# Kernel optimization log

Measured on AMD Instinct MI355X. Metric: run time of the kernel, lower is better.

The kernel has to match this reference:

```python
import jax, jax.numpy as jnp
import numpy as np

EPS = 1e-06
B, N, D, K, C = 16, 256, 4, 10, 100  # batch, nodes, pseudo dim, kernels, out_channels


def setup_inputs() -> dict:
    key = jax.random.key(0)
    k1, k2, k3, k4, k5, k6 = jax.random.split(key, 6)
    stdv = np.sqrt(6.0 / (K + D))
    x = jax.random.normal(k1, (B, N, K * C), dtype=jnp.float32)
    adj = (jax.random.uniform(k2, (B, N, N)) > 0.5).astype(jnp.float32)
    pseudo = jax.random.uniform(k3, (B, N, N, D), dtype=jnp.float32)
    mu = jax.random.uniform(k4, (K, D), minval=-stdv, maxval=stdv, dtype=jnp.float32)
    sigma = jax.random.uniform(k5, (K, D), minval=-stdv, maxval=stdv, dtype=jnp.float32)
    lim = 1.0 / np.sqrt(C)
    W = jax.random.uniform(k6, (C, C), minval=-lim, maxval=lim, dtype=jnp.float32)
    b = jnp.zeros((C,), dtype=jnp.float32)
    return {"x": x, "adj": adj, "pseudo": pseudo, "mu": mu, "sigma": sigma, "W": W, "b": b}


def reference(x, adj, pseudo, mu, sigma, W, b):
    # Gaussian kernel edge weights: [B,N,N,K]
    diff = pseudo[..., None, :] - mu            # [B,N,N,K,D]
    g = jnp.exp(jnp.sum(-0.5 * diff ** 2 / (EPS + sigma ** 2), axis=-1))
    ag = g * adj[..., None]                     # adjacency-masked weights [B,N,N,K]
    xk = x.reshape(B, N, K, C) @ W.T + b        # per-kernel linear  [B,N,K,C]
    # res[b,k,c,n] = sum_m ag[b,n,m,k] * xk[b,m,k,c]
    res = jnp.einsum('bnmk,bmkc->bkcn', ag, xk)
    return res.reshape(B, K * C, N)
```

## Files before the change

kernel.cpp:

```cpp
#include <hip/hip_runtime.h>

typedef __bf16 bf16;
typedef __attribute__((ext_vector_type(4)))  __bf16 bf16x4;
typedef __attribute__((ext_vector_type(8)))  __bf16 bf16x8;
typedef __attribute__((ext_vector_type(4)))  float  f32x4;
typedef __attribute__((ext_vector_type(16))) float  f32x16;

constexpr int B_ = 16, N_ = 256, K_ = 10, C_ = 100, CP_ = 112;
constexpr float NL2E = -0.7213475204444817f;
constexpr int BF_SLICE = 16 * 2 * 128 * 8;

__device__ inline bf16x8 cvt8(const float* p) {
    float4 a = *(const float4*)p, b = *(const float4*)(p + 4);
    bf16x8 r = {(bf16)a.x, (bf16)a.y, (bf16)a.z, (bf16)a.w,
                (bf16)b.x, (bf16)b.y, (bf16)b.z, (bf16)b.w};
    return r;
}
__device__ inline bf16x8 cvt4z(const float* p) {
    float4 a = *(const float4*)p;
    bf16x8 r = {(bf16)a.x, (bf16)a.y, (bf16)a.z, (bf16)a.w,
                (bf16)0.0f, (bf16)0.0f, (bf16)0.0f, (bf16)0.0f};
    return r;
}

__global__ __launch_bounds__(256, 4) void xk_gemm(
    const float* __restrict__ x, const float* __restrict__ W,
    const float* __restrict__ bias, bf16* __restrict__ xkT)
{
    __shared__ float xs[32 * 101 + 16];

    const int bid = blockIdx.x;
    const int xcd = bid & 7, s = bid >> 3;
    const int b  = xcd + 8 * (s / 80);
    const int rr = s % 80, kk = rr >> 3, mq = rr & 7;
    const int tid = threadIdx.x;
    const int w = tid >> 6, l = tid & 63, l31 = l & 31, h = l >> 5;
    const int c = w * 32 + l31;

    const float* xb = x + ((size_t)(b * N_ + mq * 32) * K_ + kk) * C_;
    #pragma unroll 4
    for (int idx = tid; idx < 800; idx += 256) {
        int row = idx / 25, q = idx - row * 25;
        float4 v = *(const float4*)(xb + (size_t)row * (K_ * C_) + q * 4);
        *(float4*)(&xs[row * 101 + q * 4]) = v;
    }

    const bf16x8 zf = {(bf16)0.f,(bf16)0.f,(bf16)0.f,(bf16)0.f,
                       (bf16)0.f,(bf16)0.f,(bf16)0.f,(bf16)0.f};

    bf16x8 af[7];
    const float* Wrow = W + (size_t)c * C_;
    #pragma unroll
    for (int js = 0; js < 7; ++js) {
        const int jb = js * 16 + h * 8;
        af[js] = zf;
        if (c < C_) {
            if (jb + 8 <= C_)      af[js] = cvt8(Wrow + jb);
            else if (jb < C_)      af[js] = cvt4z(Wrow + jb);
        }
    }

    f32x16 acc;
    #pragma unroll
    for (int r = 0; r < 16; ++r) {
        int crow = w * 32 + (r & 3) + 8 * (r >> 2) + 4 * h;
        acc[r] = (crow < C_) ? bias[crow] : 0.0f;
    }

    __syncthreads();

    #pragma unroll
    for (int js = 0; js < 7; ++js) {
        const int jb = js * 16 + h * 8;
        bf16x8 b0 = zf;
        if (jb < C_) b0 = cvt8(&xs[l31 * 101 + jb]);
        acc = __builtin_amdgcn_mfma_f32_32x32x16_bf16(af[js], b0, acc, 0, 0, 0);
    }

    bf16* op = xkT + (size_t)(b * K_ + kk) * BF_SLICE;
    const int mg = mq * 32 + l31;
    const int base = (((mg >> 4) << 1) + ((mg >> 3) & 1)) * 1024 + (mg & 7);
    #pragma unroll
    for (int r = 0; r < 16; ++r) {
        const int crow = w * 32 + (r & 3) + 8 * (r >> 2) + 4 * h;
        op[base + crow * 8] = (bf16)acc[r];
    }
}

__global__ __launch_bounds__(256, 4) void gauss_agg(
    const float* __restrict__ adj, const float* __restrict__ pseudo,
    const float* __restrict__ mu, const float* __restrict__ sigma,
    const bf16* __restrict__ xkT, float* __restrict__ out)
{
    __shared__ __align__(16) char lds[32 * 512];

    const int bid = blockIdx.x;
    const int xcd = bid & 7, s = bid >> 3;
    const int b  = xcd + 8 * (s / 80);
    const int rr = s % 80, kk = rr >> 3, nh = rr & 7;
    const int n32 = nh * 32;
    const int tid = threadIdx.x;
    const int w = tid >> 6, l = tid & 63, l31 = l & 31, h = l >> 5;

    float Av[4], Bv[4], ga = 0.0f;
    #pragma unroll
    for (int d = 0; d < 4; ++d) {
        float sg = sigma[kk * 4 + d];
        float al = NL2E / (1e-6f + sg * sg);
        float mv = mu[kk * 4 + d];
        Av[d] = al; Bv[d] = -2.0f * al * mv; ga += al * mv * mv;
    }

    const float* pbase = pseudo + (size_t)(b * N_ + n32) * N_ * 4;
    const float* abase = adj    + (size_t)(b * N_ + n32) * N_;
    #pragma unroll
    for (int i = 0; i < 8; ++i) {
        const int row = i * 4 + w;
        const float4* pr = (const float4*)(pbase + (size_t)row * N_ * 4);
        const float*  ar = abase + (size_t)row * N_;
        float4 p0 = pr[l];
        float4 p1 = pr[l + 64];
        float4 p2 = pr[l + 128];
        float4 p3 = pr[l + 192];
        float a0 = ar[l], a1 = ar[l + 64], a2 = ar[l + 128], a3 = ar[l + 192];

        float s0 = ga + Av[0]*p0.x*p0.x + Bv[0]*p0.x + Av[1]*p0.y*p0.y + Bv[1]*p0.y
                      + Av[2]*p0.z*p0.z + Bv[2]*p0.z + Av[3]*p0.w*p0.w + Bv[3]*p0.w;
        float s1 = ga + Av[0]*p1.x*p1.x + Bv[0]*p1.x + Av[1]*p1.y*p1.y + Bv[1]*p1.y
                      + Av[2]*p1.z*p1.z + Bv[2]*p1.z + Av[3]*p1.w*p1.w + Bv[3]*p1.w;
        float s2 = ga + Av[0]*p2.x*p2.x + Bv[0]*p2.x + Av[1]*p2.y*p2.y + Bv[1]*p2.y
                      + Av[2]*p2.z*p2.z + Bv[2]*p2.z + Av[3]*p2.w*p2.w + Bv[3]*p2.w;
        float s3 = ga + Av[0]*p3.x*p3.x + Bv[0]*p3.x + Av[1]*p3.y*p3.y + Bv[1]*p3.y
                      + Av[2]*p3.z*p3.z + Bv[2]*p3.z + Av[3]*p3.w*p3.w + Bv[3]*p3.w;

        float g0 = __builtin_amdgcn_exp2f(s0) * a0;
        float g1 = __builtin_amdgcn_exp2f(s1) * a1;
        float g2 = __builtin_amdgcn_exp2f(s2) * a2;
        float g3 = __builtin_amdgcn_exp2f(s3) * a3;

        #pragma unroll
        for (int t = 0; t < 4; ++t) {
            const int m  = l + 64 * t;
            const int ch = m >> 3, half = (m >> 2) & 1, pos = m & 3;
            const float gv = (t == 0) ? g0 : (t == 1) ? g1 : (t == 2) ? g2 : g3;
            *(bf16*)(lds + row * 512 + ((ch ^ (row & 7)) * 16) + half * 8 + pos * 2)
                = (bf16)gv;
        }
    }
    __syncthreads();

    const bf16* bsl = xkT + (size_t)(b * K_ + kk) * BF_SLICE
                          + (size_t)(w * 32 + l31) * 8;
    f32x16 acc;
    #pragma unroll
    for (int i = 0; i < 16; ++i) acc[i] = 0.0f;

    #pragma unroll
    for (int ks = 0; ks < 16; ++ks) {
        bf16x8 af = *(const bf16x8*)(lds + l31 * 512 + (((ks * 2 + h) ^ (l31 & 7)) * 16));
        bf16x8 bf = *(const bf16x8*)(bsl + (size_t)(ks * 2 + h) * 1024);
        acc = __builtin_amdgcn_mfma_f32_32x32x16_bf16(af, bf, acc, 0, 0, 0);
    }

    const int c = w * 32 + l31;
    if (c < C_) {
        float* ob = out + (size_t)(b * K_ + kk) * C_ * N_ + (size_t)c * N_ + n32;
        #pragma unroll
        for (int q = 0; q < 4; ++q) {
            float4 v = {acc[4*q+0], acc[4*q+1], acc[4*q+2], acc[4*q+3]};
            *(float4*)(ob + 8 * q + 4 * h) = v;
        }
    }
}

extern "C" void kernel_launch(void* const* d_in, const int* in_sizes, int n_in,
                              void* d_out, int out_size, void* d_ws, size_t ws_size,
                              hipStream_t stream)
{
    const float* x      = (const float*)d_in[0];
    const float* adj    = (const float*)d_in[1];
    const float* pseudo = (const float*)d_in[2];
    const float* mu     = (const float*)d_in[3];
    const float* sigma  = (const float*)d_in[4];
    const float* W      = (const float*)d_in[5];
    const float* bias   = (const float*)d_in[6];
    float* out = (float*)d_out;
    bf16* xkT  = (bf16*)d_ws;

    hipLaunchKernelGGL(xk_gemm, dim3(1280), dim3(256), 0, stream, x, W, bias, xkT);
    hipLaunchKernelGGL(gauss_agg, dim3(1280), dim3(256), 0, stream,
                       adj, pseudo, mu, sigma, xkT, out);
}
```

Baseline: 33.62 us.

## Process two Gaussian kernels per block in gauss_agg to reuse pseudo/adj loads

Each gauss_agg block now handles two kernel indices (k and k+5), so the pseudo and adj tiles are loaded once and used for both weight matrices, with two LDS buffers and two MFMA accumulators. The grid halves to 640 blocks and the launch bound drops to 2 blocks per SM. This cuts redundant global reads of the large pseudo tensor. In exchange it uses more registers and LDS per block and launches fewer blocks, which lowers parallelism.

```diff
diff --git a/kernel.cpp b/kernel.cpp
--- a/kernel.cpp
+++ b/kernel.cpp
@@ -87,28 +87,32 @@
     }
 }
 
-__global__ __launch_bounds__(256, 4) void gauss_agg(
+__global__ __launch_bounds__(256, 2) void gauss_agg(
     const float* __restrict__ adj, const float* __restrict__ pseudo,
     const float* __restrict__ mu, const float* __restrict__ sigma,
     const bf16* __restrict__ xkT, float* __restrict__ out)
 {
-    __shared__ __align__(16) char lds[32 * 512];
+    __shared__ __align__(16) char lds0[32 * 512];
+    __shared__ __align__(16) char lds1[32 * 512];
 
     const int bid = blockIdx.x;
     const int xcd = bid & 7, s = bid >> 3;
-    const int b  = xcd + 8 * (s / 80);
-    const int rr = s % 80, kk = rr >> 3, nh = rr & 7;
+    const int b  = xcd + 8 * (s / 40);
+    const int rr = s % 40, kp = rr >> 3, nh = rr & 7;
+    const int k0 = kp, k1 = kp + 5;
     const int n32 = nh * 32;
     const int tid = threadIdx.x;
     const int w = tid >> 6, l = tid & 63, l31 = l & 31, h = l >> 5;
 
-    float Av[4], Bv[4], ga = 0.0f;
+    float A0[4], B0[4], g0c = 0.0f, A1[4], B1[4], g1c = 0.0f;
     #pragma unroll
     for (int d = 0; d < 4; ++d) {
-        float sg = sigma[kk * 4 + d];
-        float al = NL2E / (1e-6f + sg * sg);
-        float mv = mu[kk * 4 + d];
-        Av[d] = al; Bv[d] = -2.0f * al * mv; ga += al * mv * mv;
+        float sg0 = sigma[k0 * 4 + d], mv0 = mu[k0 * 4 + d];
+        float al0 = NL2E / (1e-6f + sg0 * sg0);
+        A0[d] = al0; B0[d] = -2.0f * al0 * mv0; g0c += al0 * mv0 * mv0;
+        float sg1 = sigma[k1 * 4 + d], mv1 = mu[k1 * 4 + d];
+        float al1 = NL2E / (1e-6f + sg1 * sg1);
+        A1[d] = al1; B1[d] = -2.0f * al1 * mv1; g1c += al1 * mv1 * mv1;
     }
 
     const float* pbase = pseudo + (size_t)(b * N_ + n32) * N_ * 4;
@@ -124,51 +128,70 @@
         float4 p3 = pr[l + 192];
         float a0 = ar[l], a1 = ar[l + 64], a2 = ar[l + 128], a3 = ar[l + 192];
 
-        float s0 = ga + Av[0]*p0.x*p0.x + Bv[0]*p0.x + Av[1]*p0.y*p0.y + Bv[1]*p0.y
-                      + Av[2]*p0.z*p0.z + Bv[2]*p0.z + Av[3]*p0.w*p0.w + Bv[3]*p0.w;
-        float s1 = ga + Av[0]*p1.x*p1.x + Bv[0]*p1.x + Av[1]*p1.y*p1.y + Bv[1]*p1.y
-                      + Av[2]*p1.z*p1.z + Bv[2]*p1.z + Av[3]*p1.w*p1.w + Bv[3]*p1.w;
-        float s2 = ga + Av[0]*p2.x*p2.x + Bv[0]*p2.x + Av[1]*p2.y*p2.y + Bv[1]*p2.y
-                      + Av[2]*p2.z*p2.z + Bv[2]*p2.z + Av[3]*p2.w*p2.w + Bv[3]*p2.w;
-        float s3 = ga + Av[0]*p3.x*p3.x + Bv[0]*p3.x + Av[1]*p3.y*p3.y + Bv[1]*p3.y
-                      + Av[2]*p3.z*p3.z + Bv[2]*p3.z + Av[3]*p3.w*p3.w + Bv[3]*p3.w;
-
-        float g0 = __builtin_amdgcn_exp2f(s0) * a0;
-        float g1 = __builtin_amdgcn_exp2f(s1) * a1;
-        float g2 = __builtin_amdgcn_exp2f(s2) * a2;
-        float g3 = __builtin_amdgcn_exp2f(s3) * a3;
+        float q0x = p0.x*p0.x, q0y = p0.y*p0.y, q0z = p0.z*p0.z, q0w = p0.w*p0.w;
+        float q1x = p1.x*p1.x, q1y = p1.y*p1.y, q1z = p1.z*p1.z, q1w = p1.w*p1.w;
+        float q2x = p2.x*p2.x, q2y = p2.y*p2.y, q2z = p2.z*p2.z, q2w = p2.w*p2.w;
+        float q3x = p3.x*p3.x, q3y = p3.y*p3.y, q3z = p3.z*p3.z, q3w = p3.w*p3.w;
+
+        float s00 = g0c + A0[0]*q0x + B0[0]*p0.x + A0[1]*q0y + B0[1]*p0.y
+                        + A0[2]*q0z + B0[2]*p0.z + A0[3]*q0w + B0[3]*p0.w;
+        float s01 = g0c + A0[0]*q1x + B0[0]*p1.x + A0[1]*q1y + B0[1]*p1.y
+                        + A0[2]*q1z + B0[2]*p1.z + A0[3]*q1w + B0[3]*p1.w;
+        float s02 = g0c + A0[0]*q2x + B0[0]*p2.x + A0[1]*q2y + B0[1]*p2.y
+                        + A0[2]*q2z + B0[2]*p2.z + A0[3]*q2w + B0[3]*p2.w;
+        float s03 = g0c + A0[0]*q3x + B0[0]*p3.x + A0[1]*q3y + B0[1]*p3.y
+                        + A0[2]*q3z + B0[2]*p3.z + A0[3]*q3w + B0[3]*p3.w;
+
+        float s10 = g1c + A1[0]*q0x + B1[0]*p0.x + A1[1]*q0y + B1[1]*p0.y
+                        + A1[2]*q0z + B1[2]*p0.z + A1[3]*q0w + B1[3]*p0.w;
+        float s11 = g1c + A1[0]*q1x + B1[0]*p1.x + A1[1]*q1y + B1[1]*p1.y
+                        + A1[2]*q1z + B1[2]*p1.z + A1[3]*q1w + B1[3]*p1.w;
+        float s12 = g1c + A1[0]*q2x + B1[0]*p2.x + A1[1]*q2y + B1[1]*p2.y
+                        + A1[2]*q2z + B1[2]*p2.z + A1[3]*q2w + B1[3]*p2.w;
+        float s13 = g1c + A1[0]*q3x + B1[0]*p3.x + A1[1]*q3y + B1[1]*p3.y
+                        + A1[2]*q3z + B1[2]*p3.z + A1[3]*q3w + B1[3]*p3.w;
 
         #pragma unroll
         for (int t = 0; t < 4; ++t) {
             const int m  = l + 64 * t;
             const int ch = m >> 3, half = (m >> 2) & 1, pos = m & 3;
-            const float gv = (t == 0) ? g0 : (t == 1) ? g1 : (t == 2) ? g2 : g3;
-            *(bf16*)(lds + row * 512 + ((ch ^ (row & 7)) * 16) + half * 8 + pos * 2)
-                = (bf16)gv;
+            const int off = row * 512 + ((ch ^ (row & 7)) * 16) + half * 8 + pos * 2;
+            const float av = (t == 0) ? a0 : (t == 1) ? a1 : (t == 2) ? a2 : a3;
+            const float sA = (t == 0) ? s00 : (t == 1) ? s01 : (t == 2) ? s02 : s03;
+            const float sB = (t == 0) ? s10 : (t == 1) ? s11 : (t == 2) ? s12 : s13;
+            *(bf16*)(lds0 + off) = (bf16)(__builtin_amdgcn_exp2f(sA) * av);
+            *(bf16*)(lds1 + off) = (bf16)(__builtin_amdgcn_exp2f(sB) * av);
         }
     }
     __syncthreads();
 
-    const bf16* bsl = xkT + (size_t)(b * K_ + kk) * BF_SLICE
-                          + (size_t)(w * 32 + l31) * 8;
-    f32x16 acc;
-    #pragma unroll
-    for (int i = 0; i < 16; ++i) acc[i] = 0.0f;
+    const bf16* bsl0 = xkT + (size_t)(b * K_ + k0) * BF_SLICE + (size_t)(w * 32 + l31) * 8;
+    const bf16* bsl1 = xkT + (size_t)(b * K_ + k1) * BF_SLICE + (size_t)(w * 32 + l31) * 8;
+    f32x16 acc0, acc1;
+    #pragma unroll
+    for (int i = 0; i < 16; ++i) { acc0[i] = 0.0f; acc1[i] = 0.0f; }
 
     #pragma unroll
     for (int ks = 0; ks < 16; ++ks) {
-        bf16x8 af = *(const bf16x8*)(lds + l31 * 512 + (((ks * 2 + h) ^ (l31 & 7)) * 16));
-        bf16x8 bf = *(const bf16x8*)(bsl + (size_t)(ks * 2 + h) * 1024);
-        acc = __builtin_amdgcn_mfma_f32_32x32x16_bf16(af, bf, acc, 0, 0, 0);
+        const int aoff = l31 * 512 + (((ks * 2 + h) ^ (l31 & 7)) * 16);
+        bf16x8 af0 = *(const bf16x8*)(lds0 + aoff);
+        bf16x8 af1 = *(const bf16x8*)(lds1 + aoff);
+        bf16x8 bf0 = *(const bf16x8*)(bsl0 + (size_t)(ks * 2 + h) * 1024);
+        bf16x8 bf1 = *(const bf16x8*)(bsl1 + (size_t)(ks * 2 + h) * 1024);
+        acc0 = __builtin_amdgcn_mfma_f32_32x32x16_bf16(af0, bf0, acc0, 0, 0, 0);
+        acc1 = __builtin_amdgcn_mfma_f32_32x32x16_bf16(af1, bf1, acc1, 0, 0, 0);
     }
 
     const int c = w * 32 + l31;
     if (c < C_) {
-        float* ob = out + (size_t)(b * K_ + kk) * C_ * N_ + (size_t)c * N_ + n32;
+        float* ob0 = out + (size_t)(b * K_ + k0) * C_ * N_ + (size_t)c * N_ + n32;
+        float* ob1 = out + (size_t)(b * K_ + k1) * C_ * N_ + (size_t)c * N_ + n32;
         #pragma unroll
         for (int q = 0; q < 4; ++q) {
-            float4 v = {acc[4*q+0], acc[4*q+1], acc[4*q+2], acc[4*q+3]};
-            *(float4*)(ob + 8 * q + 4 * h) = v;
+            float4 v0 = {acc0[4*q+0], acc0[4*q+1], acc0[4*q+2], acc0[4*q+3]};
+            float4 v1 = {acc1[4*q+0], acc1[4*q+1], acc1[4*q+2], acc1[4*q+3]};
+            *(float4*)(ob0 + 8 * q + 4 * h) = v0;
+            *(float4*)(ob1 + 8 * q + 4 * h) = v1;
         }
     }
 }
@@ -188,6 +211,6 @@
     bf16* xkT  = (bf16*)d_ws;
 
     hipLaunchKernelGGL(xk_gemm, dim3(1280), dim3(256), 0, stream, x, W, bias, xkT);
-    hipLaunchKernelGGL(gauss_agg, dim3(1280), dim3(256), 0, stream,
+    hipLaunchKernelGGL(gauss_agg, dim3(640), dim3(256), 0, stream,
                        adj, pseudo, mu, sigma, xkT, out);
 }
```

New measurement: 34.40 us. 2.3% more time.

## Fuse per-kernel linear projection into Gaussian aggregation kernel

Applied to the files above, without the earlier changes.

Merges the xk GEMM and the Gaussian-weighted aggregation into one kernel. Each block now recomputes the projected x tile for all 256 source nodes in shared memory, chunk by chunk, and consumes it right away. This removes the global bf16 intermediate and the second launch. In exchange, the projection and the x reads are repeated 8x across node-tile blocks, and two barriers are added per chunk.

```diff
diff --git a/kernel.cpp b/kernel.cpp
--- a/kernel.cpp
+++ b/kernel.cpp
@@ -6,9 +6,8 @@
 typedef __attribute__((ext_vector_type(4)))  float  f32x4;
 typedef __attribute__((ext_vector_type(16))) float  f32x16;
 
-constexpr int B_ = 16, N_ = 256, K_ = 10, C_ = 100, CP_ = 112;
+constexpr int B_ = 16, N_ = 256, K_ = 10, C_ = 100;
 constexpr float NL2E = -0.7213475204444817f;
-constexpr int BF_SLICE = 16 * 2 * 128 * 8;
 
 __device__ inline bf16x8 cvt8(const float* p) {
     float4 a = *(const float4*)p, b = *(const float4*)(p + 4);
@@ -23,27 +22,24 @@
     return r;
 }
 
-__global__ __launch_bounds__(256, 4) void xk_gemm(
-    const float* __restrict__ x, const float* __restrict__ W,
-    const float* __restrict__ bias, bf16* __restrict__ xkT)
+__global__ __launch_bounds__(256, 4) void fused_gauss(
+    const float* __restrict__ x, const float* __restrict__ adj,
+    const float* __restrict__ pseudo, const float* __restrict__ mu,
+    const float* __restrict__ sigma, const float* __restrict__ W,
+    const float* __restrict__ bias, float* __restrict__ out)
 {
     __shared__ float xs[32 * 101 + 16];
+    __shared__ bf16  xkc[4 * 128 * 8];
+    __shared__ __align__(16) char agb[32 * 512];
 
     const int bid = blockIdx.x;
     const int xcd = bid & 7, s = bid >> 3;
     const int b  = xcd + 8 * (s / 80);
-    const int rr = s % 80, kk = rr >> 3, mq = rr & 7;
+    const int rr = s % 80, kk = rr >> 3, nh = rr & 7;
+    const int n32 = nh * 32;
     const int tid = threadIdx.x;
     const int w = tid >> 6, l = tid & 63, l31 = l & 31, h = l >> 5;
     const int c = w * 32 + l31;
-
-    const float* xb = x + ((size_t)(b * N_ + mq * 32) * K_ + kk) * C_;
-    #pragma unroll 4
-    for (int idx = tid; idx < 800; idx += 256) {
-        int row = idx / 25, q = idx - row * 25;
-        float4 v = *(const float4*)(xb + (size_t)row * (K_ * C_) + q * 4);
-        *(float4*)(&xs[row * 101 + q * 4]) = v;
-    }
 
     const bf16x8 zf = {(bf16)0.f,(bf16)0.f,(bf16)0.f,(bf16)0.f,
                        (bf16)0.f,(bf16)0.f,(bf16)0.f,(bf16)0.f};
@@ -59,48 +55,12 @@
             else if (jb < C_)      af[js] = cvt4z(Wrow + jb);
         }
     }
-
-    f32x16 acc;
+    float bv[16];
     #pragma unroll
     for (int r = 0; r < 16; ++r) {
         int crow = w * 32 + (r & 3) + 8 * (r >> 2) + 4 * h;
-        acc[r] = (crow < C_) ? bias[crow] : 0.0f;
+        bv[r] = (crow < C_) ? bias[crow] : 0.0f;
     }
-
-    __syncthreads();
-
-    #pragma unroll
-    for (int js = 0; js < 7; ++js) {
-        const int jb = js * 16 + h * 8;
-        bf16x8 b0 = zf;
-        if (jb < C_) b0 = cvt8(&xs[l31 * 101 + jb]);
-        acc = __builtin_amdgcn_mfma_f32_32x32x16_bf16(af[js], b0, acc, 0, 0, 0);
-    }
-
-    bf16* op = xkT + (size_t)(b * K_ + kk) * BF_SLICE;
-    const int mg = mq * 32 + l31;
-    const int base = (((mg >> 4) << 1) + ((mg >> 3) & 1)) * 1024 + (mg & 7);
-    #pragma unroll
-    for (int r = 0; r < 16; ++r) {
-        const int crow = w * 32 + (r & 3) + 8 * (r >> 2) + 4 * h;
-        op[base + crow * 8] = (bf16)acc[r];
-    }
-}
-
-__global__ __launch_bounds__(256, 4) void gauss_agg(
-    const float* __restrict__ adj, const float* __restrict__ pseudo,
-    const float* __restrict__ mu, const float* __restrict__ sigma,
-    const bf16* __restrict__ xkT, float* __restrict__ out)
-{
-    __shared__ __align__(16) char lds[32 * 512];
-
-    const int bid = blockIdx.x;
-    const int xcd = bid & 7, s = bid >> 3;
-    const int b  = xcd + 8 * (s / 80);
-    const int rr = s % 80, kk = rr >> 3, nh = rr & 7;
-    const int n32 = nh * 32;
-    const int tid = threadIdx.x;
-    const int w = tid >> 6, l = tid & 63, l31 = l & 31, h = l >> 5;
 
     float Av[4], Bv[4], ga = 0.0f;
     #pragma unroll
@@ -143,31 +103,61 @@
             const int m  = l + 64 * t;
             const int ch = m >> 3, half = (m >> 2) & 1, pos = m & 3;
             const float gv = (t == 0) ? g0 : (t == 1) ? g1 : (t == 2) ? g2 : g3;
-            *(bf16*)(lds + row * 512 + ((ch ^ (row & 7)) * 16) + half * 8 + pos * 2)
+            *(bf16*)(agb + row * 512 + ((ch ^ (row & 7)) * 16) + half * 8 + pos * 2)
                 = (bf16)gv;
         }
     }
+
+    f32x16 acc2;
+    #pragma unroll
+    for (int i = 0; i < 16; ++i) acc2[i] = 0.0f;
+
     __syncthreads();
 
-    const bf16* bsl = xkT + (size_t)(b * K_ + kk) * BF_SLICE
-                          + (size_t)(w * 32 + l31) * 8;
-    f32x16 acc;
-    #pragma unroll
-    for (int i = 0; i < 16; ++i) acc[i] = 0.0f;
+    #pragma unroll 1
+    for (int it = 0; it < 8; ++it) {
+        const float* xb = x + ((size_t)(b * N_ + it * 32) * K_ + kk) * C_;
+        #pragma unroll 4
+        for (int idx = tid; idx < 800; idx += 256) {
+            int row = idx / 25, q = idx - row * 25;
+            float4 v = *(const float4*)(xb + (size_t)row * (K_ * C_) + q * 4);
+            *(float4*)(&xs[row * 101 + q * 4]) = v;
+        }
+        __syncthreads();
 
-    #pragma unroll
-    for (int ks = 0; ks < 16; ++ks) {
-        bf16x8 af = *(const bf16x8*)(lds + l31 * 512 + (((ks * 2 + h) ^ (l31 & 7)) * 16));
-        bf16x8 bf = *(const bf16x8*)(bsl + (size_t)(ks * 2 + h) * 1024);
-        acc = __builtin_amdgcn_mfma_f32_32x32x16_bf16(af, bf, acc, 0, 0, 0);
+        f32x16 acc;
+        #pragma unroll
+        for (int r = 0; r < 16; ++r) acc[r] = bv[r];
+        #pragma unroll
+        for (int js = 0; js < 7; ++js) {
+            const int jb = js * 16 + h * 8;
+            bf16x8 b0 = zf;
+            if (jb < C_) b0 = cvt8(&xs[l31 * 101 + jb]);
+            acc = __builtin_amdgcn_mfma_f32_32x32x16_bf16(af[js], b0, acc, 0, 0, 0);
+        }
+        const int base = (((l31 >> 4) << 1) + ((l31 >> 3) & 1)) * 1024 + (l31 & 7);
+        #pragma unroll
+        for (int r = 0; r < 16; ++r) {
+            const int crow = w * 32 + (r & 3) + 8 * (r >> 2) + 4 * h;
+            xkc[base + crow * 8] = (bf16)acc[r];
+        }
+        __syncthreads();
+
+        #pragma unroll
+        for (int ksl = 0; ksl < 2; ++ksl) {
+            const int ksg = it * 2 + ksl;
+            bf16x8 a8 = *(const bf16x8*)(agb + l31 * 512
+                          + (((ksg * 2 + h) ^ (l31 & 7)) * 16));
+            bf16x8 b8 = *(const bf16x8*)(&xkc[(ksl * 2 + h) * 1024 + c * 8]);
+            acc2 = __builtin_amdgcn_mfma_f32_32x32x16_bf16(a8, b8, acc2, 0, 0, 0);
+        }
     }
 
-    const int c = w * 32 + l31;
     if (c < C_) {
         float* ob = out + (size_t)(b * K_ + kk) * C_ * N_ + (size_t)c * N_ + n32;
         #pragma unroll
         for (int q = 0; q < 4; ++q) {
-            float4 v = {acc[4*q+0], acc[4*q+1], acc[4*q+2], acc[4*q+3]};
+            float4 v = {acc2[4*q+0], acc2[4*q+1], acc2[4*q+2], acc2[4*q+3]};
             *(float4*)(ob + 8 * q + 4 * h) = v;
         }
     }
@@ -185,9 +175,7 @@
     const float* W      = (const float*)d_in[5];
     const float* bias   = (const float*)d_in[6];
     float* out = (float*)d_out;
-    bf16* xkT  = (bf16*)d_ws;
 
-    hipLaunchKernelGGL(xk_gemm, dim3(1280), dim3(256), 0, stream, x, W, bias, xkT);
-    hipLaunchKernelGGL(gauss_agg, dim3(1280), dim3(256), 0, stream,
-                       adj, pseudo, mu, sigma, xkT, out);
+    hipLaunchKernelGGL(fused_gauss, dim3(B_ * K_ * 8), dim3(256), 0, stream,
+                       x, adj, pseudo, mu, sigma, W, bias, out);
 }
```

After: 74.79 us. 122% more time.
